# Performance work log

Hardware: AMD Instinct MI355X
Metric: run time of the kernel (lower is better)

Reference implementation:

```python
import jax, jax.numpy as jnp
import numpy as np

B, L, SRC_DIM = 64, 384, 512
HID, EMB = 512, 256
NUM_CLASSES = 250
NUM_STEPS = 127  # batch_max_length(128) - 1


def setup_inputs() -> dict:
    key = jax.random.key(0)
    ks = jax.random.split(key, 13)
    s = 0.05
    return {
        "src": jax.random.normal(ks[0], (B, L, SRC_DIM), jnp.float32),
        "text": jax.random.randint(ks[1], (B, NUM_STEPS), 0, NUM_CLASSES + 1),
        "emb_table": jax.random.normal(ks[2], (NUM_CLASSES + 1, EMB), jnp.float32) * s,
        "Wi2h": jax.random.normal(ks[3], (HID, SRC_DIM), jnp.float32) * s,
        "Wh2h": jax.random.normal(ks[4], (HID, HID), jnp.float32) * s,
        "bh2h": jax.random.normal(ks[5], (HID,), jnp.float32) * s,
        "wscore": jax.random.normal(ks[6], (HID,), jnp.float32) * s,
        "W_ih": jax.random.normal(ks[7], (4 * HID, SRC_DIM + EMB), jnp.float32) * s,
        "b_ih": jax.random.normal(ks[8], (4 * HID,), jnp.float32) * s,
        "W_hh": jax.random.normal(ks[9], (4 * HID, HID), jnp.float32) * s,
        "b_hh": jax.random.normal(ks[10], (4 * HID,), jnp.float32) * s,
        "Wgen": jax.random.normal(ks[11], (NUM_CLASSES, HID), jnp.float32) * s,
        "bgen": jax.random.normal(ks[12], (NUM_CLASSES,), jnp.float32) * s,
    }


def reference(src, text, emb_table, Wi2h, Wh2h, bh2h, wscore,
              W_ih, b_ih, W_hh, b_hh, Wgen, bgen):
    """ASTERDecoder teacher-forced forward (num_layers=1).
    src: [B, L, C]; text: [B, T] int tokens. Returns probs [B, T, num_classes].
    """
    b = src.shape[0]
    H = Wh2h.shape[0]
    # i2h(src) is constant across decode steps -> hoist out of the loop.
    src_feat = jnp.einsum('blc,hc->blh', src, Wi2h)          # [B, L, H]
    emb_seq = emb_table[text]                                # [B, T, E]

    def step(carry, emb_t):
        h, c = carry                                         # [B, H] each
        proj = h @ Wh2h.T + bh2h                             # h2h(prev_hidden)
        # Bahdanau score + softmax over L, then context via weighted sum.
        logit = jnp.tanh(src_feat + proj[:, None, :]) @ wscore   # [B, L]
        alpha = jax.nn.softmax(logit, axis=1)
        context = jnp.einsum('bl,blc->bc', alpha, src)       # [B, C]
        x = jnp.concatenate([context, emb_t], axis=1)        # [B, C+E]
        # LSTMCell gates (PyTorch order: i, f, g, o)
        gates = x @ W_ih.T + b_ih + h @ W_hh.T + b_hh        # [B, 4H]
        i, f, g, o = jnp.split(gates, 4, axis=1)
        i, f, o = jax.nn.sigmoid(i), jax.nn.sigmoid(f), jax.nn.sigmoid(o)
        g = jnp.tanh(g)
        c_new = f * c + i * g
        h_new = o * jnp.tanh(c_new)
        return (h_new, c_new), h_new

    init = (jnp.zeros((b, H), src.dtype), jnp.zeros((b, H), src.dtype))
    _, hs = jax.lax.scan(step, init, jnp.swapaxes(emb_seq, 0, 1))  # hs: [T, B, H]
    output_hiddens = jnp.swapaxes(hs, 0, 1)                  # [B, T, H]
    probs = jnp.einsum('bth,nh->btn', output_hiddens, Wgen) + bgen
    return probs
```

## Files before the change

### kernel.cpp

```cpp
#include <hip/hip_runtime.h>

typedef unsigned short u16;
typedef unsigned int   u32;
typedef _Float16 f16;
typedef f16   f16x2 __attribute__((ext_vector_type(2)));
typedef f16   f16x8 __attribute__((ext_vector_type(8)));
typedef float f32x4 __attribute__((ext_vector_type(4)));
typedef u32   u32x4 __attribute__((ext_vector_type(4)));

#define B_  64
#define L_  384
#define CS  512
#define H_  512
#define E_  256
#define NC  250
#define T_  127
#define XROW 1024

__device__ __forceinline__ float h2f(u16 u){ f16 h; __builtin_memcpy(&h,&u,2); return (float)h; }
__device__ __forceinline__ u16  f2h(float f){ f16 h=(f16)f; u16 u; __builtin_memcpy(&u,&h,2); return u; }
__device__ __forceinline__ float wredsum(float v){
#pragma unroll
  for (int o=32;o>0;o>>=1) v += __shfl_down(v, o, 64);
  return v;
}
__device__ __forceinline__ float tanh_f(float x){
  x = fminf(fmaxf(x, -15.f), 15.f);
  float e = __expf(2.f*x);
  return (e-1.f)/(e+1.f);
}
__device__ __forceinline__ float sigm_f(float x){
  x = fminf(fmaxf(x, -30.f), 30.f);
  return 1.f/(1.f+__expf(-x));
}
__device__ __forceinline__ float dot2f(u32 a, u32 b, float c){
  f16x2 x, y; __builtin_memcpy(&x,&a,4); __builtin_memcpy(&y,&b,4);
#if __has_builtin(__builtin_amdgcn_fdot2)
  return __builtin_amdgcn_fdot2(x, y, c, false);
#else
  return c + (float)x[0]*(float)y[0] + (float)x[1]*(float)y[1];
#endif
}

__global__ __launch_bounds__(256) void k_cvt(const float* __restrict__ in, f16* __restrict__ o, int n){
  int i = blockIdx.x*256 + threadIdx.x;
  if (i < n) o[i] = (f16)in[i];
}

__global__ __launch_bounds__(256) void k_packwhq(const float* __restrict__ Wh, u32* __restrict__ Wq){
  int i = blockIdx.x*256 + threadIdx.x;
  if (i < 64*512*4){
    int kq = i >> 11, n = (i >> 2) & 511, e = i & 3;
    int k = kq*8 + e*2;
    u32 lo = f2h(Wh[(size_t)n*512 + k]);
    u32 hi = f2h(Wh[(size_t)n*512 + k + 1]);
    Wq[i] = lo | (hi<<16);
  }
}

__global__ __launch_bounds__(256) void k_packwg(const float* __restrict__ Wih,
    const float* __restrict__ Whh, const float* __restrict__ bih, const float* __restrict__ bhh,
    f16* __restrict__ Wg, float* __restrict__ bias_g){
  int i = blockIdx.x*256 + threadIdx.x;
  if (i < 2048*1280){
    int p = i / 1280, c = i - p*1280;
    int j = p >> 4, q = p & 15, g = q >> 2, hl = q & 3;
    int r = g*512 + (j<<2) + hl;
    float v = (c < 768) ? Wih[(size_t)r*768 + c] : Whh[(size_t)r*512 + (c-768)];
    Wg[i] = (f16)v;
    if (c == 0) bias_g[p] = bih[r] + bhh[r];
  }
}

__global__ __launch_bounds__(256) void k_emb(const int* __restrict__ text,
    const float* __restrict__ embt, f16* __restrict__ embseq){
  int i = blockIdx.x*256 + threadIdx.x;
  if (i < B_*T_*E_){
    int bt = i >> 8, col = i & 255;
    int tok = text[bt];
    embseq[i] = (f16)embt[(size_t)tok*E_ + col];
  }
}

__global__ __launch_bounds__(256) void k_sf_mfma(
    const float* __restrict__ A, const f16* __restrict__ Wn, u16* __restrict__ sf)
{
  int w = threadIdx.x >> 6, lane = threadIdx.x & 63;
  int quad = lane >> 4, l16 = lane & 15;
  int m0 = blockIdx.x * 64;
  int nb = blockIdx.y * 256 + w * 64;
  const float* ap0 = A  + (size_t)(m0 + l16)*512 + quad*8;
  const f16*   bp0 = Wn + (size_t)(nb + l16)*512 + quad*8;
  f32x4 acc[4][4] = {};
  for (int k0=0; k0<512; k0+=32){
    f16x8 bfr[4];
#pragma unroll
    for (int nt=0; nt<4; nt++)
      bfr[nt] = *(const f16x8*)(bp0 + (size_t)nt*16*512 + k0);
#pragma unroll
    for (int f=0; f<4; f++){
      const float* ap = ap0 + (size_t)f*16*512 + k0;
      float4 a0 = *(const float4*)ap;
      float4 a1 = *(const float4*)(ap+4);
      f16x8 afr = { (f16)a0.x,(f16)a0.y,(f16)a0.z,(f16)a0.w,
                    (f16)a1.x,(f16)a1.y,(f16)a1.z,(f16)a1.w };
#pragma unroll
      for (int nt=0; nt<4; nt++)
        acc[f][nt] = __builtin_amdgcn_mfma_f32_16x16x32_f16(afr, bfr[nt], acc[f][nt], 0,0,0);
    }
  }
#pragma unroll
  for (int f=0; f<4; f++)
#pragma unroll
    for (int nt=0; nt<4; nt++)
#pragma unroll
      for (int r=0; r<4; r++){
        int m = m0 + f*16 + quad*4 + r;
        int n = nb + nt*16 + l16;
        sf[(size_t)m*512 + n] = f2h(acc[f][nt][r]);
      }
}

__global__ __launch_bounds__(256) void gemm_probs(
    const u16* __restrict__ A, const float* __restrict__ W, const float* __restrict__ bias,
    float* __restrict__ Cd, int M, int N, int K)
{
  __shared__ float As[16][64+1];
  __shared__ float Ws[16][64+1];
  const int tid = threadIdx.x;
  const int bm = blockIdx.x*64, bn = blockIdx.y*64;
  const int lr = tid>>2;
  const int lc = (tid&3)*4;
  const int ty = tid>>4, tx = tid&15;
  float acc[4][4];
#pragma unroll
  for (int i=0;i<4;i++)
#pragma unroll
    for (int j=0;j<4;j++) acc[i][j]=0.f;

  for (int k0=0;k0<K;k0+=16){
    ushort4 va = *(const ushort4*)(A + (size_t)(bm+lr)*K + k0 + lc);
    As[lc+0][lr]=h2f(va.x); As[lc+1][lr]=h2f(va.y); As[lc+2][lr]=h2f(va.z); As[lc+3][lr]=h2f(va.w);
    int n = bn + lr;
    if (n < N){
      float4 vw = *(const float4*)(W + (size_t)n*K + k0 + lc);
      Ws[lc+0][lr]=vw.x; Ws[lc+1][lr]=vw.y; Ws[lc+2][lr]=vw.z; Ws[lc+3][lr]=vw.w;
    } else {
      Ws[lc+0][lr]=0.f; Ws[lc+1][lr]=0.f; Ws[lc+2][lr]=0.f; Ws[lc+3][lr]=0.f;
    }
    __syncthreads();
#pragma unroll
    for (int k=0;k<16;k++){
      float a[4], w[4];
#pragma unroll
      for (int i=0;i<4;i++) a[i]=As[k][ty*4+i];
#pragma unroll
      for (int j=0;j<4;j++) w[j]=Ws[k][tx*4+j];
#pragma unroll
      for (int i=0;i<4;i++)
#pragma unroll
        for (int j=0;j<4;j++) acc[i][j] += a[i]*w[j];
    }
    __syncthreads();
  }
#pragma unroll
  for (int i=0;i<4;i++){
    int m = bm + ty*4 + i;
#pragma unroll
    for (int j=0;j<4;j++){
      int n = bn + tx*4 + j;
      if (n < N) Cd[(size_t)m*N + n] = acc[i][j] + bias[n];
    }
  }
}

__global__ __launch_bounds__(512) void k_att1(
    const u32* __restrict__ WhQ, const u16* __restrict__ sf,
    const f16* __restrict__ Xc, const float* __restrict__ bh2h,
    const float* __restrict__ wsc, float* __restrict__ logit)
{
  const int b   = blockIdx.x >> 2;
  const int q   = blockIdx.x & 3;
  const int tid = threadIdx.x;
  const int wid = tid >> 6, lane = tid & 63;

  __shared__ __align__(16) u32 sh_h2[256];
  __shared__ float sh_proj[512];

  if (tid < 256) sh_h2[tid] = ((const u32*)(Xc + (size_t)b*XROW + 512))[tid];
  __syncthreads();

  {
    const u32* wp = WhQ + ((size_t)tid << 2);
    const u32x4* hp = (const u32x4*)sh_h2;
    float a0=0.f, a1=0.f, a2=0.f, a3=0.f;
#pragma unroll 8
    for (int kq=0; kq<64; kq++){
      u32x4 wq = *(const u32x4*)(wp + ((size_t)kq << 11));
      u32x4 hq = hp[kq];
      a0 = dot2f(wq.x, hq.x, a0);
      a1 = dot2f(wq.y, hq.y, a1);
      a2 = dot2f(wq.z, hq.z, a2);
      a3 = dot2f(wq.w, hq.w, a3);
    }
    sh_proj[tid] = (a0+a1) + (a2+a3) + bh2h[tid];
  }
  __syncthreads();

  {
    float pv[8], wv[8];
#pragma unroll
    for (int j=0;j<8;j++){ pv[j]=sh_proj[lane*8+j]; wv[j]=wsc[lane*8+j]; }
    const int l0 = q*96 + wid*12;
    const f16* sp0 = (const f16*)sf + (((size_t)(b*L_ + l0)) << 9) + lane*8;
#pragma unroll 4
    for (int i=0;i<12;i++){
      f16x8 s = *(const f16x8*)(sp0 + ((size_t)i << 9));
      float v;
      v  = tanh_f((float)s[0]+pv[0])*wv[0];
      v += tanh_f((float)s[1]+pv[1])*wv[1];
      v += tanh_f((float)s[2]+pv[2])*wv[2];
      v += tanh_f((float)s[3]+pv[3])*wv[3];
      v += tanh_f((float)s[4]+pv[4])*wv[4];
      v += tanh_f((float)s[5]+pv[5])*wv[5];
      v += tanh_f((float)s[6]+pv[6])*wv[6];
      v += tanh_f((float)s[7]+pv[7])*wv[7];
      v = wredsum(v);
      if (lane == 0) logit[b*L_ + l0 + i] = v;
    }
  }
}

__global__ __launch_bounds__(512) void k_ctx2(
    const float* __restrict__ logit, const f16* __restrict__ src16,
    f16* __restrict__ Xc)
{
  const int b   = blockIdx.x;
  const int tid = threadIdx.x;
  const int wid = tid >> 6, lane = tid & 63;

  __shared__ float sh_al[L_];
  __shared__ float sh_red[16];
  __shared__ float sh_cp[8][512];

  float inv;
  {
    float va = (tid < L_) ? logit[b*L_ + tid] : -3.0e38f;
    float m = va;
#pragma unroll
    for (int o=32;o>0;o>>=1) m = fmaxf(m, __shfl_down(m,o,64));
    if (lane==0) sh_red[wid] = m;
    __syncthreads();
    m = fmaxf(fmaxf(fmaxf(sh_red[0],sh_red[1]),fmaxf(sh_red[2],sh_red[3])),
              fmaxf(fmaxf(sh_red[4],sh_red[5]),fmaxf(sh_red[6],sh_red[7])));
    float e = (tid < L_) ? __expf(va - m) : 0.f;
    if (tid < L_) sh_al[tid] = e;
    float ss = wredsum(e);
    if (lane==0) sh_red[8+wid] = ss;
    __syncthreads();
    inv = 1.f/(((sh_red[8]+sh_red[9])+(sh_red[10]+sh_red[11]))
             + ((sh_red[12]+sh_red[13])+(sh_red[14]+sh_red[15])));
  }

  {
    float acc[8] = {0.f,0.f,0.f,0.f,0.f,0.f,0.f,0.f};
    const f16* sp0 = src16 + (((size_t)(b*L_ + wid*48)) << 9) + lane*8;
    const float* alp = sh_al + wid*48;
#pragma unroll 4
    for (int i=0;i<48;i++){
      f16x8 v = *(const f16x8*)(sp0 + ((size_t)i << 9));
      float al = alp[i];
#pragma unroll
      for (int e=0;e<8;e++) acc[e] += al*(float)v[e];
    }
#pragma unroll
    for (int e=0;e<8;e++) sh_cp[wid][lane*8+e] = acc[e];
  }
  __syncthreads();
  if (tid < 256){
    int c0 = tid*2;
    float v0 = (((sh_cp[0][c0]+sh_cp[1][c0])+(sh_cp[2][c0]+sh_cp[3][c0]))
              + ((sh_cp[4][c0]+sh_cp[5][c0])+(sh_cp[6][c0]+sh_cp[7][c0])))*inv;
    int c1 = c0+1;
    float v1 = (((sh_cp[0][c1]+sh_cp[1][c1])+(sh_cp[2][c1]+sh_cp[3][c1]))
              + ((sh_cp[4][c1]+sh_cp[5][c1])+(sh_cp[6][c1]+sh_cp[7][c1])))*inv;
    u32 o = (u32)f2h(v0) | ((u32)f2h(v1) << 16);
    ((u32*)(Xc + (size_t)b*XROW))[tid] = o;
  }
}

__global__ __launch_bounds__(256) void k_gates(
    const f16* __restrict__ X, const f16* __restrict__ Wg,
    const float* __restrict__ bias_g, const f16* __restrict__ embseq,
    float* __restrict__ cbuf, f16* __restrict__ Xn, u16* __restrict__ hs, int t)
{
  __shared__ float gbuf[64][17];
  const int tid  = threadIdx.x;
  const int wid  = tid >> 6, lane = tid & 63;
  const int quad = lane >> 4, l16 = lane & 15;
  const int j = blockIdx.x;
  const f16* bp   = Wg + (size_t)(j*16 + l16)*1280 + quad*8;
  const int brow  = wid*16 + l16;
  const f16* actx = X + (size_t)brow*XROW + quad*8;
  const f16* aemb = embseq + (((size_t)brow*T_ + t)<<8) + quad*8;
  const f16* ah   = actx + 512;
  f32x4 acc = {};
#pragma unroll
  for (int k0=0;k0<512;k0+=32)
    acc = __builtin_amdgcn_mfma_f32_16x16x32_f16(*(const f16x8*)(actx+k0), *(const f16x8*)(bp+k0), acc, 0,0,0);
#pragma unroll
  for (int k0=0;k0<256;k0+=32)
    acc = __builtin_amdgcn_mfma_f32_16x16x32_f16(*(const f16x8*)(aemb+k0), *(const f16x8*)(bp+512+k0), acc, 0,0,0);
#pragma unroll
  for (int k0=0;k0<512;k0+=32)
    acc = __builtin_amdgcn_mfma_f32_16x16x32_f16(*(const f16x8*)(ah+k0), *(const f16x8*)(bp+768+k0), acc, 0,0,0);
#pragma unroll
  for (int r=0;r<4;r++) gbuf[wid*16 + quad*4 + r][l16] = acc[r];
  __syncthreads();
  const int b = tid >> 2, hl = tid & 3;
  const int hd = j*4 + hl;
  float gi = gbuf[b][ 0+hl] + bias_g[j*16 +  0 + hl];
  float gf = gbuf[b][ 4+hl] + bias_g[j*16 +  4 + hl];
  float gg = gbuf[b][ 8+hl] + bias_g[j*16 +  8 + hl];
  float go = gbuf[b][12+hl] + bias_g[j*16 + 12 + hl];
  float fi=sigm_f(gi), ff=sigm_f(gf), fg=tanh_f(gg), fo=sigm_f(go);
  size_t ci = ((size_t)b<<9) + hd;
  float cn = ff*cbuf[ci] + fi*fg;
  float hn = fo*tanh_f(cn);
  cbuf[ci] = cn;
  Xn[(size_t)b*XROW + 512 + hd] = (f16)hn;
  hs[(((size_t)(b*T_ + t))<<9) + hd] = f2h(hn);
}

extern "C" void kernel_launch(void* const* d_in, const int* in_sizes, int n_in,
                              void* d_out, int out_size, void* d_ws, size_t ws_size,
                              hipStream_t stream)
{
  const float* src   = (const float*)d_in[0];
  const int*   text  = (const int*)d_in[1];
  const float* embt  = (const float*)d_in[2];
  const float* Wi2h  = (const float*)d_in[3];
  const float* Wh2h  = (const float*)d_in[4];
  const float* bh2h  = (const float*)d_in[5];
  const float* wsc   = (const float*)d_in[6];
  const float* W_ih  = (const float*)d_in[7];
  const float* b_ih  = (const float*)d_in[8];
  const float* W_hh  = (const float*)d_in[9];
  const float* b_hh  = (const float*)d_in[10];
  const float* Wgen  = (const float*)d_in[11];
  const float* bgen  = (const float*)d_in[12];
  float* out = (float*)d_out;

  char* p = (char*)d_ws;
  u16*   sfw    = (u16*)p;    p += (size_t)B_*L_*H_*2;
  u16*   hsw    = (u16*)p;    p += (size_t)B_*T_*H_*2;
  f16*   src16  = (f16*)p;    p += (size_t)B_*L_*CS*2;
  u32*   WhQ    = (u32*)p;    p += (size_t)64*512*4*4;
  f16*   Wi2h16 = (f16*)p;    p += (size_t)H_*CS*2;
  f16*   WgF    = (f16*)p;    p += (size_t)2048*1280*2;
  f16*   embseq = (f16*)p;    p += (size_t)B_*T_*E_*2;
  f16*   X0     = (f16*)p;    p += (size_t)B_*XROW*2;
  f16*   X1     = (f16*)p;    p += (size_t)B_*XROW*2;
  float* logitw = (float*)p;  p += (size_t)B_*L_*4;
  float* cbuf   = (float*)p;  p += (size_t)B_*H_*4;
  float* bias_g = (float*)p;  p += (size_t)2048*4;

  hipMemsetAsync(X0,   0, (size_t)B_*XROW*2*2, stream);
  hipMemsetAsync(cbuf, 0, (size_t)B_*H_*4, stream);

  k_cvt    <<<(H_*CS+255)/256,    256, 0, stream>>>(Wi2h, Wi2h16, H_*CS);
  k_cvt    <<<(B_*L_*CS+255)/256, 256, 0, stream>>>(src, src16, B_*L_*CS);
  k_packwhq<<<(64*512*4+255)/256, 256, 0, stream>>>(Wh2h, WhQ);
  k_packwg <<<(2048*1280+255)/256,256, 0, stream>>>(W_ih, W_hh, b_ih, b_hh, WgF, bias_g);
  k_emb    <<<(B_*T_*E_+255)/256, 256, 0, stream>>>(text, embt, embseq);

  k_sf_mfma<<<dim3(384,2), 256, 0, stream>>>(src, Wi2h16, sfw);

  for (int t=0; t<T_; t++){
    f16* Xc = (t & 1) ? X1 : X0;
    f16* Xn = (t & 1) ? X0 : X1;
    k_att1<<<256, 512, 0, stream>>>(WhQ, sfw, Xc, bh2h, wsc, logitw);
    k_ctx2<<<64, 512, 0, stream>>>(logitw, src16, Xc);
    k_gates<<<128, 256, 0, stream>>>(Xc, WgF, bias_g, embseq, cbuf, Xn, hsw, t);
  }

  dim3 g2(B_*T_/64, (NC+63)/64);
  gemm_probs<<<g2, 256, 0, stream>>>(hsw, Wgen, bgen, out, B_*T_, NC, H_);
}
```

Before: 5.016 ms.

## Precompute src@W_ih context projection and fuse step into two kernels

Uses linearity to precompute src projected through the context part of W_ih (a [B,L,2048] f16 tensor), so each step's context contribution to the gates becomes an alpha-weighted sum over that tensor instead of a context vector followed by a GEMM. The h/embedding gate part is computed by extra MFMA blocks inside the attention-logit kernel, which cuts the per-step launches from three to two. In exchange each step streams a 100MB precomputed tensor (four times the src bytes) and needs a much larger workspace, with a fallback to the old path when the workspace is too small.

```diff
diff --git a/kernel.cpp b/kernel.cpp
--- a/kernel.cpp
+++ b/kernel.cpp
@@ -16,6 +16,7 @@
 #define NC  250
 #define T_  127
 #define XROW 1024
+#define XEH  768
 
 __device__ __forceinline__ float h2f(u16 u){ f16 h; __builtin_memcpy(&h,&u,2); return (float)h; }
 __device__ __forceinline__ u16  f2h(float f){ f16 h=(f16)f; u16 u; __builtin_memcpy(&u,&h,2); return u; }
@@ -55,6 +56,28 @@
     u32 lo = f2h(Wh[(size_t)n*512 + k]);
     u32 hi = f2h(Wh[(size_t)n*512 + k + 1]);
     Wq[i] = lo | (hi<<16);
+  }
+}
+
+__global__ __launch_bounds__(256) void k_packwcp(const float* __restrict__ Wih, f16* __restrict__ Wcp){
+  int i = blockIdx.x*256 + threadIdx.x;
+  if (i < 2048*512){
+    int pc = i >> 9, k = i & 511;
+    int r = (pc&3)*512 + (pc>>2);
+    Wcp[i] = (f16)Wih[(size_t)r*768 + k];
+  }
+}
+
+__global__ __launch_bounds__(256) void k_packwgp2(const float* __restrict__ Wih,
+    const float* __restrict__ Whh, const float* __restrict__ bih, const float* __restrict__ bhh,
+    f16* __restrict__ WgP, float* __restrict__ bias_g){
+  int i = blockIdx.x*256 + threadIdx.x;
+  if (i < 2048*768){
+    int pc = i / 768, k = i - pc*768;
+    int r = (pc&3)*512 + (pc>>2);
+    float v = (k < 256) ? Wih[(size_t)r*768 + 512 + k] : Whh[(size_t)r*512 + (k-256)];
+    WgP[i] = (f16)v;
+    if (k == 0) bias_g[pc] = bih[r] + bhh[r];
   }
 }
 
@@ -82,8 +105,13 @@
   }
 }
 
+__global__ __launch_bounds__(128) void k_initeh(const f16* __restrict__ embseq, f16* __restrict__ Xeh){
+  int b = blockIdx.x, tid = threadIdx.x;
+  ((u32*)(Xeh + (size_t)b*XEH))[tid] = ((const u32*)(embseq + ((size_t)(b*T_))*256))[tid];
+}
+
 __global__ __launch_bounds__(256) void k_sf_mfma(
-    const float* __restrict__ A, const f16* __restrict__ Wn, u16* __restrict__ sf)
+    const float* __restrict__ A, const f16* __restrict__ Wn, u16* __restrict__ Cd, int N)
 {
   int w = threadIdx.x >> 6, lane = threadIdx.x & 63;
   int quad = lane >> 4, l16 = lane & 15;
@@ -117,7 +145,7 @@
       for (int r=0; r<4; r++){
         int m = m0 + f*16 + quad*4 + r;
         int n = nb + nt*16 + l16;
-        sf[(size_t)m*512 + n] = f2h(acc[f][nt][r]);
+        Cd[(size_t)m*N + n] = f2h(acc[f][nt][r]);
       }
 }
 
@@ -174,6 +202,157 @@
   }
 }
 
+__global__ __launch_bounds__(512) void k_step1(
+    const u32* __restrict__ WhQ, const u16* __restrict__ sf,
+    const f16* __restrict__ Xeh, const float* __restrict__ bh2h,
+    const float* __restrict__ wsc, float* __restrict__ logit,
+    const f16* __restrict__ WgP, const float* __restrict__ bias_g,
+    float* __restrict__ gpart)
+{
+  const int tid = threadIdx.x;
+  const int wid = tid >> 6, lane = tid & 63;
+  __shared__ __align__(16) u32 sh_h2[256];
+  __shared__ float sh_proj[512];
+
+  if (blockIdx.x < 256){
+    const int b = blockIdx.x >> 2;
+    const int q = blockIdx.x & 3;
+    if (tid < 256) sh_h2[tid] = ((const u32*)(Xeh + (size_t)b*XEH + 256))[tid];
+    __syncthreads();
+    {
+      const u32* wp = WhQ + ((size_t)tid << 2);
+      const u32x4* hp = (const u32x4*)sh_h2;
+      float a0=0.f, a1=0.f, a2=0.f, a3=0.f;
+#pragma unroll 8
+      for (int kq=0; kq<64; kq++){
+        u32x4 wq = *(const u32x4*)(wp + ((size_t)kq << 11));
+        u32x4 hq = hp[kq];
+        a0 = dot2f(wq.x, hq.x, a0);
+        a1 = dot2f(wq.y, hq.y, a1);
+        a2 = dot2f(wq.z, hq.z, a2);
+        a3 = dot2f(wq.w, hq.w, a3);
+      }
+      sh_proj[tid] = (a0+a1) + (a2+a3) + bh2h[tid];
+    }
+    __syncthreads();
+    {
+      float pv[8], wv[8];
+#pragma unroll
+      for (int j=0;j<8;j++){ pv[j]=sh_proj[lane*8+j]; wv[j]=wsc[lane*8+j]; }
+      const int l0 = q*96 + wid*12;
+      const f16* sp0 = (const f16*)sf + (((size_t)(b*L_ + l0)) << 9) + lane*8;
+#pragma unroll 4
+      for (int i=0;i<12;i++){
+        f16x8 s = *(const f16x8*)(sp0 + ((size_t)i << 9));
+        float v;
+        v  = tanh_f((float)s[0]+pv[0])*wv[0];
+        v += tanh_f((float)s[1]+pv[1])*wv[1];
+        v += tanh_f((float)s[2]+pv[2])*wv[2];
+        v += tanh_f((float)s[3]+pv[3])*wv[3];
+        v += tanh_f((float)s[4]+pv[4])*wv[4];
+        v += tanh_f((float)s[5]+pv[5])*wv[5];
+        v += tanh_f((float)s[6]+pv[6])*wv[6];
+        v += tanh_f((float)s[7]+pv[7])*wv[7];
+        v = wredsum(v);
+        if (lane == 0) logit[b*L_ + l0 + i] = v;
+      }
+    }
+  } else {
+    const int j = blockIdx.x - 256;
+    const int quad = lane >> 4, l16 = lane & 15;
+    const int n = j*128 + wid*16 + l16;
+    const f16* bp  = WgP + (size_t)n*768 + quad*8;
+    const f16* ap0 = Xeh + (size_t)l16*XEH + quad*8;
+    f32x4 acc[4] = {};
+    for (int k0=0; k0<768; k0+=32){
+      f16x8 bfr = *(const f16x8*)(bp + k0);
+#pragma unroll
+      for (int f=0; f<4; f++){
+        f16x8 afr = *(const f16x8*)(ap0 + (size_t)f*16*XEH + k0);
+        acc[f] = __builtin_amdgcn_mfma_f32_16x16x32_f16(afr, bfr, acc[f], 0,0,0);
+      }
+    }
+    float bias = bias_g[n];
+#pragma unroll
+    for (int f=0; f<4; f++)
+#pragma unroll
+      for (int r=0; r<4; r++){
+        int b2 = f*16 + quad*4 + r;
+        gpart[(size_t)b2*2048 + n] = acc[f][r] + bias;
+      }
+  }
+}
+
+__global__ __launch_bounds__(512) void k_step2(
+    const float* __restrict__ logit, const u16* __restrict__ sg,
+    const float* __restrict__ gpart, const f16* __restrict__ embseq,
+    float* __restrict__ cbuf, f16* __restrict__ Xeh, u16* __restrict__ hs, int t)
+{
+  const int b = blockIdx.x >> 2, q = blockIdx.x & 3;
+  const int tid = threadIdx.x;
+  const int wid = tid >> 6, lane = tid & 63;
+  __shared__ float sh_al[L_];
+  __shared__ float sh_red[16];
+  __shared__ float sh_gs[2][512];
+
+  float inv;
+  {
+    float va = (tid < L_) ? logit[b*L_ + tid] : -3.0e38f;
+    float m = va;
+#pragma unroll
+    for (int o=32;o>0;o>>=1) m = fmaxf(m, __shfl_down(m,o,64));
+    if (lane==0) sh_red[wid] = m;
+    __syncthreads();
+    m = fmaxf(fmaxf(fmaxf(sh_red[0],sh_red[1]),fmaxf(sh_red[2],sh_red[3])),
+              fmaxf(fmaxf(sh_red[4],sh_red[5]),fmaxf(sh_red[6],sh_red[7])));
+    float e = (tid < L_) ? __expf(va - m) : 0.f;
+    if (tid < L_) sh_al[tid] = e;
+    float ss = wredsum(e);
+    if (lane==0) sh_red[8+wid] = ss;
+    __syncthreads();
+    inv = 1.f/(((sh_red[8]+sh_red[9])+(sh_red[10]+sh_red[11]))
+             + ((sh_red[12]+sh_red[13])+(sh_red[14]+sh_red[15])));
+  }
+
+  {
+    const int cp = tid & 255, lh = tid >> 8;
+    const u32* sp = (const u32*)sg + ((size_t)(b*L_ + lh*192))*1024 + q*256 + cp;
+    const float* alp = sh_al + lh*192;
+    float a0 = 0.f, a1 = 0.f;
+#pragma unroll 8
+    for (int l=0;l<192;l++){
+      u32 v = sp[(size_t)l*1024];
+      f16x2 p2; __builtin_memcpy(&p2,&v,4);
+      float al = alp[l];
+      a0 += al*(float)p2[0];
+      a1 += al*(float)p2[1];
+    }
+    sh_gs[lh][cp*2  ] = a0;
+    sh_gs[lh][cp*2+1] = a1;
+  }
+  __syncthreads();
+
+  if (tid < 128){
+    const float4 gp = *(const float4*)(gpart + (size_t)b*2048 + q*512 + tid*4);
+    float gi = (sh_gs[0][tid*4+0] + sh_gs[1][tid*4+0])*inv + gp.x;
+    float gf = (sh_gs[0][tid*4+1] + sh_gs[1][tid*4+1])*inv + gp.y;
+    float gg = (sh_gs[0][tid*4+2] + sh_gs[1][tid*4+2])*inv + gp.z;
+    float go = (sh_gs[0][tid*4+3] + sh_gs[1][tid*4+3])*inv + gp.w;
+    float fi=sigm_f(gi), ff=sigm_f(gf), fg=tanh_f(gg), fo=sigm_f(go);
+    const int hd = q*128 + tid;
+    size_t ci = ((size_t)b<<9) + hd;
+    float cn = ff*cbuf[ci] + fi*fg;
+    float hn = fo*tanh_f(cn);
+    cbuf[ci] = cn;
+    Xeh[(size_t)b*XEH + 256 + hd] = (f16)hn;
+    hs[((size_t)(b*T_ + t))*512 + hd] = f2h(hn);
+  } else if (q == 0 && tid >= 256 && tid < 384 && (t+1) < T_){
+    int c = tid - 256;
+    ((u32*)(Xeh + (size_t)b*XEH))[c] =
+        ((const u32*)(embseq + ((size_t)(b*T_ + t + 1))*256))[c];
+  }
+}
+
 __global__ __launch_bounds__(512) void k_att1(
     const u32* __restrict__ WhQ, const u16* __restrict__ sf,
     const f16* __restrict__ Xc, const float* __restrict__ bh2h,
@@ -183,13 +362,10 @@
   const int q   = blockIdx.x & 3;
   const int tid = threadIdx.x;
   const int wid = tid >> 6, lane = tid & 63;
-
   __shared__ __align__(16) u32 sh_h2[256];
   __shared__ float sh_proj[512];
-
   if (tid < 256) sh_h2[tid] = ((const u32*)(Xc + (size_t)b*XROW + 512))[tid];
   __syncthreads();
-
   {
     const u32* wp = WhQ + ((size_t)tid << 2);
     const u32x4* hp = (const u32x4*)sh_h2;
@@ -206,7 +382,6 @@
     sh_proj[tid] = (a0+a1) + (a2+a3) + bh2h[tid];
   }
   __syncthreads();
-
   {
     float pv[8], wv[8];
 #pragma unroll
@@ -238,11 +413,9 @@
   const int b   = blockIdx.x;
   const int tid = threadIdx.x;
   const int wid = tid >> 6, lane = tid & 63;
-
   __shared__ float sh_al[L_];
   __shared__ float sh_red[16];
   __shared__ float sh_cp[8][512];
-
   float inv;
   {
     float va = (tid < L_) ? logit[b*L_ + tid] : -3.0e38f;
@@ -261,7 +434,6 @@
     inv = 1.f/(((sh_red[8]+sh_red[9])+(sh_red[10]+sh_red[11]))
              + ((sh_red[12]+sh_red[13])+(sh_red[14]+sh_red[15])));
   }
-
   {
     float acc[8] = {0.f,0.f,0.f,0.f,0.f,0.f,0.f,0.f};
     const f16* sp0 = src16 + (((size_t)(b*L_ + wid*48)) << 9) + lane*8;
@@ -351,39 +523,81 @@
   const float* bgen  = (const float*)d_in[12];
   float* out = (float*)d_out;
 
-  char* p = (char*)d_ws;
-  u16*   sfw    = (u16*)p;    p += (size_t)B_*L_*H_*2;
-  u16*   hsw    = (u16*)p;    p += (size_t)B_*T_*H_*2;
-  f16*   src16  = (f16*)p;    p += (size_t)B_*L_*CS*2;
-  u32*   WhQ    = (u32*)p;    p += (size_t)64*512*4*4;
-  f16*   Wi2h16 = (f16*)p;    p += (size_t)H_*CS*2;
-  f16*   WgF    = (f16*)p;    p += (size_t)2048*1280*2;
-  f16*   embseq = (f16*)p;    p += (size_t)B_*T_*E_*2;
-  f16*   X0     = (f16*)p;    p += (size_t)B_*XROW*2;
-  f16*   X1     = (f16*)p;    p += (size_t)B_*XROW*2;
-  float* logitw = (float*)p;  p += (size_t)B_*L_*4;
-  float* cbuf   = (float*)p;  p += (size_t)B_*H_*4;
-  float* bias_g = (float*)p;  p += (size_t)2048*4;
-
-  hipMemsetAsync(X0,   0, (size_t)B_*XROW*2*2, stream);
-  hipMemsetAsync(cbuf, 0, (size_t)B_*H_*4, stream);
-
-  k_cvt    <<<(H_*CS+255)/256,    256, 0, stream>>>(Wi2h, Wi2h16, H_*CS);
-  k_cvt    <<<(B_*L_*CS+255)/256, 256, 0, stream>>>(src, src16, B_*L_*CS);
-  k_packwhq<<<(64*512*4+255)/256, 256, 0, stream>>>(Wh2h, WhQ);
-  k_packwg <<<(2048*1280+255)/256,256, 0, stream>>>(W_ih, W_hh, b_ih, b_hh, WgF, bias_g);
-  k_emb    <<<(B_*T_*E_+255)/256, 256, 0, stream>>>(text, embt, embseq);
-
-  k_sf_mfma<<<dim3(384,2), 256, 0, stream>>>(src, Wi2h16, sfw);
-
-  for (int t=0; t<T_; t++){
-    f16* Xc = (t & 1) ? X1 : X0;
-    f16* Xn = (t & 1) ? X0 : X1;
-    k_att1<<<256, 512, 0, stream>>>(WhQ, sfw, Xc, bh2h, wsc, logitw);
-    k_ctx2<<<64, 512, 0, stream>>>(logitw, src16, Xc);
-    k_gates<<<128, 256, 0, stream>>>(Xc, WgF, bias_g, embseq, cbuf, Xn, hsw, t);
-  }
-
-  dim3 g2(B_*T_/64, (NC+63)/64);
-  gemm_probs<<<g2, 256, 0, stream>>>(hsw, Wgen, bgen, out, B_*T_, NC, H_);
-}
+  const size_t NEED_NEW = (size_t)25165824 + 8323072 + 100663296 + 524288 + 524288
+                        + 2097152 + 3145728 + 4161536 + 98304 + 98304 + 524288
+                        + 131072 + 8192;
+
+  if (ws_size >= NEED_NEW){
+    char* p = (char*)d_ws;
+    u16*   sfw    = (u16*)p;    p += (size_t)B_*L_*H_*2;
+    u16*   hsw    = (u16*)p;    p += (size_t)B_*T_*H_*2;
+    u16*   sg     = (u16*)p;    p += (size_t)B_*L_*2048*2;
+    u32*   WhQ    = (u32*)p;    p += (size_t)64*512*4*4;
+    f16*   Wi2h16 = (f16*)p;    p += (size_t)H_*CS*2;
+    f16*   Wcp    = (f16*)p;    p += (size_t)2048*512*2;
+    f16*   WgP    = (f16*)p;    p += (size_t)2048*768*2;
+    f16*   embseq = (f16*)p;    p += (size_t)B_*T_*E_*2;
+    f16*   Xeh    = (f16*)p;    p += (size_t)B_*XEH*2;
+    float* logitw = (float*)p;  p += (size_t)B_*L_*4;
+    float* gpart  = (float*)p;  p += (size_t)B_*2048*4;
+    float* cbuf   = (float*)p;  p += (size_t)B_*H_*4;
+    float* bias_g = (float*)p;  p += (size_t)2048*4;
+
+    hipMemsetAsync(Xeh,  0, (size_t)B_*XEH*2, stream);
+    hipMemsetAsync(cbuf, 0, (size_t)B_*H_*4, stream);
+
+    k_cvt     <<<(H_*CS+255)/256,    256, 0, stream>>>(Wi2h, Wi2h16, H_*CS);
+    k_packwhq <<<(64*512*4+255)/256, 256, 0, stream>>>(Wh2h, WhQ);
+    k_packwcp <<<(2048*512+255)/256, 256, 0, stream>>>(W_ih, Wcp);
+    k_packwgp2<<<(2048*768+255)/256, 256, 0, stream>>>(W_ih, W_hh, b_ih, b_hh, WgP, bias_g);
+    k_emb     <<<(B_*T_*E_+255)/256, 256, 0, stream>>>(text, embt, embseq);
+    k_initeh  <<<B_, 128, 0, stream>>>(embseq, Xeh);
+
+    k_sf_mfma<<<dim3(384,2), 256, 0, stream>>>(src, Wi2h16, sfw, 512);
+    k_sf_mfma<<<dim3(384,8), 256, 0, stream>>>(src, Wcp,    sg,  2048);
+
+    for (int t=0; t<T_; t++){
+      k_step1<<<272, 512, 0, stream>>>(WhQ, sfw, Xeh, bh2h, wsc, logitw, WgP, bias_g, gpart);
+      k_step2<<<256, 512, 0, stream>>>(logitw, sg, gpart, embseq, cbuf, Xeh, hsw, t);
+    }
+
+    dim3 g2(B_*T_/64, (NC+63)/64);
+    gemm_probs<<<g2, 256, 0, stream>>>(hsw, Wgen, bgen, out, B_*T_, NC, H_);
+  } else {
+    char* p = (char*)d_ws;
+    u16*   sfw    = (u16*)p;    p += (size_t)B_*L_*H_*2;
+    u16*   hsw    = (u16*)p;    p += (size_t)B_*T_*H_*2;
+    f16*   src16  = (f16*)p;    p += (size_t)B_*L_*CS*2;
+    u32*   WhQ    = (u32*)p;    p += (size_t)64*512*4*4;
+    f16*   Wi2h16 = (f16*)p;    p += (size_t)H_*CS*2;
+    f16*   WgF    = (f16*)p;    p += (size_t)2048*1280*2;
+    f16*   embseq = (f16*)p;    p += (size_t)B_*T_*E_*2;
+    f16*   X0     = (f16*)p;    p += (size_t)B_*XROW*2;
+    f16*   X1     = (f16*)p;    p += (size_t)B_*XROW*2;
+    float* logitw = (float*)p;  p += (size_t)B_*L_*4;
+    float* cbuf   = (float*)p;  p += (size_t)B_*H_*4;
+    float* bias_g = (float*)p;  p += (size_t)2048*4;
+
+    hipMemsetAsync(X0,   0, (size_t)B_*XROW*2*2, stream);
+    hipMemsetAsync(cbuf, 0, (size_t)B_*H_*4, stream);
+
+    k_cvt    <<<(H_*CS+255)/256,    256, 0, stream>>>(Wi2h, Wi2h16, H_*CS);
+    k_cvt    <<<(B_*L_*CS+255)/256, 256, 0, stream>>>(src, src16, B_*L_*CS);
+    k_packwhq<<<(64*512*4+255)/256, 256, 0, stream>>>(Wh2h, WhQ);
+    k_packwg <<<(2048*1280+255)/256,256, 0, stream>>>(W_ih, W_hh, b_ih, b_hh, WgF, bias_g);
+    k_emb    <<<(B_*T_*E_+255)/256, 256, 0, stream>>>(text, embt, embseq);
+
+    k_sf_mfma<<<dim3(384,2), 256, 0, stream>>>(src, Wi2h16, sfw, 512);
+
+    for (int t=0; t<T_; t++){
+      f16* Xc = (t & 1) ? X1 : X0;
+      f16* Xn = (t & 1) ? X0 : X1;
+      k_att1<<<256, 512, 0, stream>>>(WhQ, sfw, Xc, bh2h, wsc, logitw);
+      k_ctx2<<<64, 512, 0, stream>>>(logitw, src16, Xc);
+      k_gates<<<128, 256, 0, stream>>>(Xc, WgF, bias_g, embseq, cbuf, Xn, hsw, t);
+    }
+
+    dim3 g2(B_*T_/64, (NC+63)/64);
+    gemm_probs<<<g2, 256, 0, stream>>>(hsw, Wgen, bgen, out, B_*T_, NC, H_);
+  }
+}
```

After: 6.815 ms. +35.9%, slower.

## Fuse attention and context per step, overlap emb/h gate GEMM, MFMA output projection

Applied to the files above, without the earlier changes.

Each decode step drops from three kernels to two. The first kernel runs score, exp and partial context per quarter of L, and in the same launch extra blocks compute the embedding and hidden gate contributions. The second reduces the partial contexts and denominators, applies the context gate GEMM and the LSTM cell. The softmax max pass is replaced by a fixed shift of 20, which removes one global reduction but relies on logits staying within a bounded range to avoid overflow or underflow. The final probability GEMM moves from a scalar fp32 tiled kernel to fp16 MFMA.

```diff
diff --git a/kernel.cpp b/kernel.cpp
--- a/kernel.cpp
+++ b/kernel.cpp
@@ -15,7 +15,7 @@
 #define E_  256
 #define NC  250
 #define T_  127
-#define XROW 1024
+#define MSHIFT 20.0f
 
 __device__ __forceinline__ float h2f(u16 u){ f16 h; __builtin_memcpy(&h,&u,2); return (float)h; }
 __device__ __forceinline__ u16  f2h(float f){ f16 h=(f16)f; u16 u; __builtin_memcpy(&u,&h,2); return u; }
@@ -58,17 +58,25 @@
   }
 }
 
-__global__ __launch_bounds__(256) void k_packwg(const float* __restrict__ Wih,
+__global__ __launch_bounds__(256) void k_packwcp(const float* __restrict__ Wih, f16* __restrict__ Wcp){
+  int i = blockIdx.x*256 + threadIdx.x;
+  if (i < 2048*512){
+    int pc = i >> 9, k = i & 511;
+    int r = (pc&3)*512 + (pc>>2);
+    Wcp[i] = (f16)Wih[(size_t)r*768 + k];
+  }
+}
+
+__global__ __launch_bounds__(256) void k_packwgp2(const float* __restrict__ Wih,
     const float* __restrict__ Whh, const float* __restrict__ bih, const float* __restrict__ bhh,
-    f16* __restrict__ Wg, float* __restrict__ bias_g){
+    f16* __restrict__ WgP, float* __restrict__ bias_g){
   int i = blockIdx.x*256 + threadIdx.x;
-  if (i < 2048*1280){
-    int p = i / 1280, c = i - p*1280;
-    int j = p >> 4, q = p & 15, g = q >> 2, hl = q & 3;
-    int r = g*512 + (j<<2) + hl;
-    float v = (c < 768) ? Wih[(size_t)r*768 + c] : Whh[(size_t)r*512 + (c-768)];
-    Wg[i] = (f16)v;
-    if (c == 0) bias_g[p] = bih[r] + bhh[r];
+  if (i < 2048*768){
+    int pc = i / 768, k = i - pc*768;
+    int r = (pc&3)*512 + (pc>>2);
+    float v = (k < 256) ? Wih[(size_t)r*768 + 512 + k] : Whh[(size_t)r*512 + (k-256)];
+    WgP[i] = (f16)v;
+    if (k == 0) bias_g[pc] = bih[r] + bhh[r];
   }
 }
 
@@ -83,7 +91,7 @@
 }
 
 __global__ __launch_bounds__(256) void k_sf_mfma(
-    const float* __restrict__ A, const f16* __restrict__ Wn, u16* __restrict__ sf)
+    const float* __restrict__ A, const f16* __restrict__ Wn, u16* __restrict__ Cd, int N)
 {
   int w = threadIdx.x >> 6, lane = threadIdx.x & 63;
   int quad = lane >> 4, l16 = lane & 15;
@@ -117,219 +125,236 @@
       for (int r=0; r<4; r++){
         int m = m0 + f*16 + quad*4 + r;
         int n = nb + nt*16 + l16;
-        sf[(size_t)m*512 + n] = f2h(acc[f][nt][r]);
-      }
-}
-
-__global__ __launch_bounds__(256) void gemm_probs(
-    const u16* __restrict__ A, const float* __restrict__ W, const float* __restrict__ bias,
-    float* __restrict__ Cd, int M, int N, int K)
+        Cd[(size_t)m*N + n] = f2h(acc[f][nt][r]);
+      }
+}
+
+__global__ __launch_bounds__(256) void k_probs_mfma(
+    const u16* __restrict__ A, const f16* __restrict__ Wn,
+    const float* __restrict__ bias, float* __restrict__ Cd)
 {
-  __shared__ float As[16][64+1];
-  __shared__ float Ws[16][64+1];
-  const int tid = threadIdx.x;
-  const int bm = blockIdx.x*64, bn = blockIdx.y*64;
-  const int lr = tid>>2;
-  const int lc = (tid&3)*4;
-  const int ty = tid>>4, tx = tid&15;
-  float acc[4][4];
-#pragma unroll
-  for (int i=0;i<4;i++)
-#pragma unroll
-    for (int j=0;j<4;j++) acc[i][j]=0.f;
-
-  for (int k0=0;k0<K;k0+=16){
-    ushort4 va = *(const ushort4*)(A + (size_t)(bm+lr)*K + k0 + lc);
-    As[lc+0][lr]=h2f(va.x); As[lc+1][lr]=h2f(va.y); As[lc+2][lr]=h2f(va.z); As[lc+3][lr]=h2f(va.w);
-    int n = bn + lr;
-    if (n < N){
-      float4 vw = *(const float4*)(W + (size_t)n*K + k0 + lc);
-      Ws[lc+0][lr]=vw.x; Ws[lc+1][lr]=vw.y; Ws[lc+2][lr]=vw.z; Ws[lc+3][lr]=vw.w;
-    } else {
-      Ws[lc+0][lr]=0.f; Ws[lc+1][lr]=0.f; Ws[lc+2][lr]=0.f; Ws[lc+3][lr]=0.f;
-    }
-    __syncthreads();
-#pragma unroll
-    for (int k=0;k<16;k++){
-      float a[4], w[4];
-#pragma unroll
-      for (int i=0;i<4;i++) a[i]=As[k][ty*4+i];
-#pragma unroll
-      for (int j=0;j<4;j++) w[j]=Ws[k][tx*4+j];
-#pragma unroll
-      for (int i=0;i<4;i++)
-#pragma unroll
-        for (int j=0;j<4;j++) acc[i][j] += a[i]*w[j];
-    }
-    __syncthreads();
-  }
-#pragma unroll
-  for (int i=0;i<4;i++){
-    int m = bm + ty*4 + i;
-#pragma unroll
-    for (int j=0;j<4;j++){
-      int n = bn + tx*4 + j;
-      if (n < N) Cd[(size_t)m*N + n] = acc[i][j] + bias[n];
-    }
-  }
-}
-
-__global__ __launch_bounds__(512) void k_att1(
+  int w = threadIdx.x >> 6, lane = threadIdx.x & 63;
+  int quad = lane >> 4, l16 = lane & 15;
+  int m0 = blockIdx.x * 64;
+  int nb = w * 64;
+  const f16* ap0 = (const f16*)A + (size_t)(m0 + l16)*512 + quad*8;
+  const f16* bp0 = Wn + (size_t)(nb + l16)*512 + quad*8;
+  f32x4 acc[4][4] = {};
+  for (int k0=0; k0<512; k0+=32){
+    f16x8 bfr[4];
+#pragma unroll
+    for (int nt=0; nt<4; nt++)
+      bfr[nt] = *(const f16x8*)(bp0 + (size_t)nt*16*512 + k0);
+#pragma unroll
+    for (int f=0; f<4; f++){
+      f16x8 afr = *(const f16x8*)(ap0 + (size_t)f*16*512 + k0);
+#pragma unroll
+      for (int nt=0; nt<4; nt++)
+        acc[f][nt] = __builtin_amdgcn_mfma_f32_16x16x32_f16(afr, bfr[nt], acc[f][nt], 0,0,0);
+    }
+  }
+#pragma unroll
+  for (int f=0; f<4; f++)
+#pragma unroll
+    for (int nt=0; nt<4; nt++)
+#pragma unroll
+      for (int r=0; r<4; r++){
+        int m = m0 + f*16 + quad*4 + r;
+        int n = nb + nt*16 + l16;
+        if (n < NC) Cd[(size_t)m*NC + n] = acc[f][nt][r] + bias[n];
+      }
+}
+
+__global__ __launch_bounds__(512) void k_stepA(
     const u32* __restrict__ WhQ, const u16* __restrict__ sf,
-    const f16* __restrict__ Xc, const float* __restrict__ bh2h,
-    const float* __restrict__ wsc, float* __restrict__ logit)
+    const f16* __restrict__ src16, const f16* __restrict__ hbuf,
+    const float* __restrict__ bh2h, const float* __restrict__ wsc,
+    const f16* __restrict__ WgP, const float* __restrict__ bias_g,
+    const f16* __restrict__ embseq,
+    float* __restrict__ ctxp, float* __restrict__ denp,
+    float* __restrict__ gpart, int t)
 {
-  const int b   = blockIdx.x >> 2;
-  const int q   = blockIdx.x & 3;
   const int tid = threadIdx.x;
   const int wid = tid >> 6, lane = tid & 63;
 
-  __shared__ __align__(16) u32 sh_h2[256];
-  __shared__ float sh_proj[512];
-
-  if (tid < 256) sh_h2[tid] = ((const u32*)(Xc + (size_t)b*XROW + 512))[tid];
-  __syncthreads();
-
-  {
-    const u32* wp = WhQ + ((size_t)tid << 2);
-    const u32x4* hp = (const u32x4*)sh_h2;
-    float a0=0.f, a1=0.f, a2=0.f, a3=0.f;
+  if (blockIdx.x < 256){
+    const int b = blockIdx.x >> 2;
+    const int q = blockIdx.x & 3;
+    __shared__ __align__(16) u32 sh_h2[256];
+    __shared__ float sh_proj[512];
+    __shared__ float sh_e[96];
+    __shared__ float sh_cp[8][512];
+
+    if (tid < 256) sh_h2[tid] = ((const u32*)(hbuf + (size_t)b*512))[tid];
+    __syncthreads();
+    {
+      const u32* wp = WhQ + ((size_t)tid << 2);
+      const u32x4* hp = (const u32x4*)sh_h2;
+      float a0=0.f, a1=0.f, a2=0.f, a3=0.f;
 #pragma unroll 8
-    for (int kq=0; kq<64; kq++){
-      u32x4 wq = *(const u32x4*)(wp + ((size_t)kq << 11));
-      u32x4 hq = hp[kq];
-      a0 = dot2f(wq.x, hq.x, a0);
-      a1 = dot2f(wq.y, hq.y, a1);
-      a2 = dot2f(wq.z, hq.z, a2);
-      a3 = dot2f(wq.w, hq.w, a3);
-    }
-    sh_proj[tid] = (a0+a1) + (a2+a3) + bh2h[tid];
-  }
-  __syncthreads();
-
-  {
-    float pv[8], wv[8];
-#pragma unroll
-    for (int j=0;j<8;j++){ pv[j]=sh_proj[lane*8+j]; wv[j]=wsc[lane*8+j]; }
-    const int l0 = q*96 + wid*12;
-    const f16* sp0 = (const f16*)sf + (((size_t)(b*L_ + l0)) << 9) + lane*8;
+      for (int kq=0; kq<64; kq++){
+        u32x4 wq = *(const u32x4*)(wp + ((size_t)kq << 11));
+        u32x4 hq = hp[kq];
+        a0 = dot2f(wq.x, hq.x, a0);
+        a1 = dot2f(wq.y, hq.y, a1);
+        a2 = dot2f(wq.z, hq.z, a2);
+        a3 = dot2f(wq.w, hq.w, a3);
+      }
+      sh_proj[tid] = (a0+a1) + (a2+a3) + bh2h[tid];
+    }
+    __syncthreads();
+    {
+      float pv[8], wv[8];
+#pragma unroll
+      for (int j=0;j<8;j++){ pv[j]=sh_proj[lane*8+j]; wv[j]=wsc[lane*8+j]; }
+      const int l0 = q*96 + wid*12;
+      const f16* sp0 = (const f16*)sf + (((size_t)(b*L_ + l0)) << 9) + lane*8;
 #pragma unroll 4
-    for (int i=0;i<12;i++){
-      f16x8 s = *(const f16x8*)(sp0 + ((size_t)i << 9));
-      float v;
-      v  = tanh_f((float)s[0]+pv[0])*wv[0];
-      v += tanh_f((float)s[1]+pv[1])*wv[1];
-      v += tanh_f((float)s[2]+pv[2])*wv[2];
-      v += tanh_f((float)s[3]+pv[3])*wv[3];
-      v += tanh_f((float)s[4]+pv[4])*wv[4];
-      v += tanh_f((float)s[5]+pv[5])*wv[5];
-      v += tanh_f((float)s[6]+pv[6])*wv[6];
-      v += tanh_f((float)s[7]+pv[7])*wv[7];
+      for (int i=0;i<12;i++){
+        f16x8 s = *(const f16x8*)(sp0 + ((size_t)i << 9));
+        float v;
+        v  = tanh_f((float)s[0]+pv[0])*wv[0];
+        v += tanh_f((float)s[1]+pv[1])*wv[1];
+        v += tanh_f((float)s[2]+pv[2])*wv[2];
+        v += tanh_f((float)s[3]+pv[3])*wv[3];
+        v += tanh_f((float)s[4]+pv[4])*wv[4];
+        v += tanh_f((float)s[5]+pv[5])*wv[5];
+        v += tanh_f((float)s[6]+pv[6])*wv[6];
+        v += tanh_f((float)s[7]+pv[7])*wv[7];
+        v = wredsum(v);
+        if (lane == 0) sh_e[wid*12 + i] = __expf(v - MSHIFT);
+      }
+    }
+    __syncthreads();
+    if (wid == 0){
+      float v = sh_e[lane] + (lane < 32 ? sh_e[64+lane] : 0.f);
       v = wredsum(v);
-      if (lane == 0) logit[b*L_ + l0 + i] = v;
-    }
-  }
-}
-
-__global__ __launch_bounds__(512) void k_ctx2(
-    const float* __restrict__ logit, const f16* __restrict__ src16,
-    f16* __restrict__ Xc)
+      if (lane == 0) denp[q*64 + b] = v;
+    }
+    {
+      float acc[8] = {0.f,0.f,0.f,0.f,0.f,0.f,0.f,0.f};
+      const f16* sp0 = src16 + (((size_t)(b*L_ + q*96 + wid*12)) << 9) + lane*8;
+      const float* alp = sh_e + wid*12;
+#pragma unroll 4
+      for (int i=0;i<12;i++){
+        f16x8 v = *(const f16x8*)(sp0 + ((size_t)i << 9));
+        float al = alp[i];
+#pragma unroll
+        for (int e=0;e<8;e++) acc[e] += al*(float)v[e];
+      }
+#pragma unroll
+      for (int e=0;e<8;e++) sh_cp[wid][lane*8+e] = acc[e];
+    }
+    __syncthreads();
+    if (tid < 256){
+      int c0 = tid*2;
+      float v0 = (((sh_cp[0][c0]+sh_cp[1][c0])+(sh_cp[2][c0]+sh_cp[3][c0]))
+                + ((sh_cp[4][c0]+sh_cp[5][c0])+(sh_cp[6][c0]+sh_cp[7][c0])));
+      int c1 = c0+1;
+      float v1 = (((sh_cp[0][c1]+sh_cp[1][c1])+(sh_cp[2][c1]+sh_cp[3][c1]))
+                + ((sh_cp[4][c1]+sh_cp[5][c1])+(sh_cp[6][c1]+sh_cp[7][c1])));
+      float2 o; o.x = v0; o.y = v1;
+      *(float2*)(ctxp + (((size_t)(q*64 + b)) << 9) + c0) = o;
+    }
+  } else {
+    const int j = blockIdx.x - 256;
+    const int quad = lane >> 4, l16 = lane & 15;
+    const int n = j*128 + wid*16 + l16;
+    const f16* bp = WgP + (size_t)n*768 + quad*8;
+    f32x4 acc[4] = {};
+    for (int k0=0; k0<256; k0+=32){
+      f16x8 bfr = *(const f16x8*)(bp + k0);
+#pragma unroll
+      for (int f=0; f<4; f++){
+        int br = f*16 + l16;
+        f16x8 afr = *(const f16x8*)(embseq + (((size_t)(br*T_ + t)) << 8) + quad*8 + k0);
+        acc[f] = __builtin_amdgcn_mfma_f32_16x16x32_f16(afr, bfr, acc[f], 0,0,0);
+      }
+    }
+    for (int k0=0; k0<512; k0+=32){
+      f16x8 bfr = *(const f16x8*)(bp + 256 + k0);
+#pragma unroll
+      for (int f=0; f<4; f++){
+        int br = f*16 + l16;
+        f16x8 afr = *(const f16x8*)(hbuf + (size_t)br*512 + quad*8 + k0);
+        acc[f] = __builtin_amdgcn_mfma_f32_16x16x32_f16(afr, bfr, acc[f], 0,0,0);
+      }
+    }
+    float bias = bias_g[n];
+#pragma unroll
+    for (int f=0; f<4; f++)
+#pragma unroll
+      for (int r=0; r<4; r++){
+        int b2 = f*16 + quad*4 + r;
+        gpart[((size_t)b2 << 11) + n] = acc[f][r] + bias;
+      }
+  }
+}
+
+__global__ __launch_bounds__(256) void k_stepB(
+    const float* __restrict__ ctxp, const float* __restrict__ denp,
+    const float* __restrict__ gpart, const f16* __restrict__ Wcp,
+    float* __restrict__ cbuf, f16* __restrict__ hbuf, u16* __restrict__ hs, int t)
 {
-  const int b   = blockIdx.x;
+  __shared__ f16   sh_ctx[64][520];
+  __shared__ float gbuf[64][17];
+  __shared__ float sh_inv[64];
   const int tid = threadIdx.x;
   const int wid = tid >> 6, lane = tid & 63;
-
-  __shared__ float sh_al[L_];
-  __shared__ float sh_red[16];
-  __shared__ float sh_cp[8][512];
-
-  float inv;
-  {
-    float va = (tid < L_) ? logit[b*L_ + tid] : -3.0e38f;
-    float m = va;
-#pragma unroll
-    for (int o=32;o>0;o>>=1) m = fmaxf(m, __shfl_down(m,o,64));
-    if (lane==0) sh_red[wid] = m;
-    __syncthreads();
-    m = fmaxf(fmaxf(fmaxf(sh_red[0],sh_red[1]),fmaxf(sh_red[2],sh_red[3])),
-              fmaxf(fmaxf(sh_red[4],sh_red[5]),fmaxf(sh_red[6],sh_red[7])));
-    float e = (tid < L_) ? __expf(va - m) : 0.f;
-    if (tid < L_) sh_al[tid] = e;
-    float ss = wredsum(e);
-    if (lane==0) sh_red[8+wid] = ss;
-    __syncthreads();
-    inv = 1.f/(((sh_red[8]+sh_red[9])+(sh_red[10]+sh_red[11]))
-             + ((sh_red[12]+sh_red[13])+(sh_red[14]+sh_red[15])));
-  }
-
-  {
-    float acc[8] = {0.f,0.f,0.f,0.f,0.f,0.f,0.f,0.f};
-    const f16* sp0 = src16 + (((size_t)(b*L_ + wid*48)) << 9) + lane*8;
-    const float* alp = sh_al + wid*48;
-#pragma unroll 4
-    for (int i=0;i<48;i++){
-      f16x8 v = *(const f16x8*)(sp0 + ((size_t)i << 9));
-      float al = alp[i];
-#pragma unroll
-      for (int e=0;e<8;e++) acc[e] += al*(float)v[e];
-    }
-#pragma unroll
-    for (int e=0;e<8;e++) sh_cp[wid][lane*8+e] = acc[e];
-  }
-  __syncthreads();
-  if (tid < 256){
-    int c0 = tid*2;
-    float v0 = (((sh_cp[0][c0]+sh_cp[1][c0])+(sh_cp[2][c0]+sh_cp[3][c0]))
-              + ((sh_cp[4][c0]+sh_cp[5][c0])+(sh_cp[6][c0]+sh_cp[7][c0])))*inv;
-    int c1 = c0+1;
-    float v1 = (((sh_cp[0][c1]+sh_cp[1][c1])+(sh_cp[2][c1]+sh_cp[3][c1]))
-              + ((sh_cp[4][c1]+sh_cp[5][c1])+(sh_cp[6][c1]+sh_cp[7][c1])))*inv;
-    u32 o = (u32)f2h(v0) | ((u32)f2h(v1) << 16);
-    ((u32*)(Xc + (size_t)b*XROW))[tid] = o;
-  }
-}
-
-__global__ __launch_bounds__(256) void k_gates(
-    const f16* __restrict__ X, const f16* __restrict__ Wg,
-    const float* __restrict__ bias_g, const f16* __restrict__ embseq,
-    float* __restrict__ cbuf, f16* __restrict__ Xn, u16* __restrict__ hs, int t)
-{
-  __shared__ float gbuf[64][17];
-  const int tid  = threadIdx.x;
-  const int wid  = tid >> 6, lane = tid & 63;
   const int quad = lane >> 4, l16 = lane & 15;
   const int j = blockIdx.x;
-  const f16* bp   = Wg + (size_t)(j*16 + l16)*1280 + quad*8;
-  const int brow  = wid*16 + l16;
-  const f16* actx = X + (size_t)brow*XROW + quad*8;
-  const f16* aemb = embseq + (((size_t)brow*T_ + t)<<8) + quad*8;
-  const f16* ah   = actx + 512;
-  f32x4 acc = {};
-#pragma unroll
-  for (int k0=0;k0<512;k0+=32)
-    acc = __builtin_amdgcn_mfma_f32_16x16x32_f16(*(const f16x8*)(actx+k0), *(const f16x8*)(bp+k0), acc, 0,0,0);
-#pragma unroll
-  for (int k0=0;k0<256;k0+=32)
-    acc = __builtin_amdgcn_mfma_f32_16x16x32_f16(*(const f16x8*)(aemb+k0), *(const f16x8*)(bp+512+k0), acc, 0,0,0);
-#pragma unroll
-  for (int k0=0;k0<512;k0+=32)
-    acc = __builtin_amdgcn_mfma_f32_16x16x32_f16(*(const f16x8*)(ah+k0), *(const f16x8*)(bp+768+k0), acc, 0,0,0);
-#pragma unroll
-  for (int r=0;r<4;r++) gbuf[wid*16 + quad*4 + r][l16] = acc[r];
+
+  if (tid < 64)
+    sh_inv[tid] = 1.f/(((denp[tid] + denp[64+tid]) + (denp[128+tid] + denp[192+tid])));
   __syncthreads();
-  const int b = tid >> 2, hl = tid & 3;
-  const int hd = j*4 + hl;
-  float gi = gbuf[b][ 0+hl] + bias_g[j*16 +  0 + hl];
-  float gf = gbuf[b][ 4+hl] + bias_g[j*16 +  4 + hl];
-  float gg = gbuf[b][ 8+hl] + bias_g[j*16 +  8 + hl];
-  float go = gbuf[b][12+hl] + bias_g[j*16 + 12 + hl];
-  float fi=sigm_f(gi), ff=sigm_f(gf), fg=tanh_f(gg), fo=sigm_f(go);
-  size_t ci = ((size_t)b<<9) + hd;
-  float cn = ff*cbuf[ci] + fi*fg;
-  float hn = fo*tanh_f(cn);
-  cbuf[ci] = cn;
-  Xn[(size_t)b*XROW + 512 + hd] = (f16)hn;
-  hs[(((size_t)(b*T_ + t))<<9) + hd] = f2h(hn);
+
+#pragma unroll 4
+  for (int i=0;i<32;i++){
+    int flat = tid + i*256;
+    int b = flat >> 7, c4 = flat & 127;
+    const float* base = ctxp + ((size_t)b << 9) + (c4 << 2);
+    float4 v0 = *(const float4*)(base);
+    float4 v1 = *(const float4*)(base + (64<<9));
+    float4 v2 = *(const float4*)(base + (128<<9));
+    float4 v3 = *(const float4*)(base + (192<<9));
+    float inv = sh_inv[b];
+    int c = c4*4;
+    sh_ctx[b][c+0] = (f16)(((v0.x+v1.x)+(v2.x+v3.x))*inv);
+    sh_ctx[b][c+1] = (f16)(((v0.y+v1.y)+(v2.y+v3.y))*inv);
+    sh_ctx[b][c+2] = (f16)(((v0.z+v1.z)+(v2.z+v3.z))*inv);
+    sh_ctx[b][c+3] = (f16)(((v0.w+v1.w)+(v2.w+v3.w))*inv);
+  }
+  __syncthreads();
+
+  {
+    const f16* bp = Wcp + (size_t)(j*16 + l16)*512 + quad*8;
+    const f16* ap = &sh_ctx[wid*16 + l16][quad*8];
+    f32x4 acc = {};
+#pragma unroll
+    for (int k0=0; k0<512; k0+=32)
+      acc = __builtin_amdgcn_mfma_f32_16x16x32_f16(*(const f16x8*)(ap + k0),
+                                                   *(const f16x8*)(bp + k0), acc, 0,0,0);
+#pragma unroll
+    for (int r=0;r<4;r++) gbuf[wid*16 + quad*4 + r][l16] = acc[r];
+  }
+  __syncthreads();
+
+  {
+    const int b2 = tid >> 2, hl = tid & 3;
+    const int hd = j*4 + hl;
+    float4 gp = *(const float4*)(gpart + ((size_t)b2 << 11) + (size_t)hd*4);
+    float gi = gbuf[b2][hl*4+0] + gp.x;
+    float gf = gbuf[b2][hl*4+1] + gp.y;
+    float gg = gbuf[b2][hl*4+2] + gp.z;
+    float go = gbuf[b2][hl*4+3] + gp.w;
+    float fi=sigm_f(gi), ff=sigm_f(gf), fg=tanh_f(gg), fo=sigm_f(go);
+    size_t ci = ((size_t)b2 << 9) + hd;
+    float cn = ff*cbuf[ci] + fi*fg;
+    float hn = fo*tanh_f(cn);
+    cbuf[ci] = cn;
+    hbuf[((size_t)b2 << 9) + hd] = (f16)hn;
+    hs[((size_t)(b2*T_ + t)) * 512 + hd] = f2h(hn);
+  }
 }
 
 extern "C" void kernel_launch(void* const* d_in, const int* in_sizes, int n_in,
@@ -357,33 +382,36 @@
   f16*   src16  = (f16*)p;    p += (size_t)B_*L_*CS*2;
   u32*   WhQ    = (u32*)p;    p += (size_t)64*512*4*4;
   f16*   Wi2h16 = (f16*)p;    p += (size_t)H_*CS*2;
-  f16*   WgF    = (f16*)p;    p += (size_t)2048*1280*2;
+  f16*   Wcp    = (f16*)p;    p += (size_t)2048*512*2;
+  f16*   WgP    = (f16*)p;    p += (size_t)2048*768*2;
+  f16*   Wgen16 = (f16*)p;    p += (size_t)256*512*2;
   f16*   embseq = (f16*)p;    p += (size_t)B_*T_*E_*2;
-  f16*   X0     = (f16*)p;    p += (size_t)B_*XROW*2;
-  f16*   X1     = (f16*)p;    p += (size_t)B_*XROW*2;
-  float* logitw = (float*)p;  p += (size_t)B_*L_*4;
+  f16*   hbuf   = (f16*)p;    p += (size_t)B_*H_*2;
+  float* ctxp   = (float*)p;  p += (size_t)4*B_*512*4;
+  float* denp   = (float*)p;  p += (size_t)256*4;
+  float* gpart  = (float*)p;  p += (size_t)B_*2048*4;
   float* cbuf   = (float*)p;  p += (size_t)B_*H_*4;
   float* bias_g = (float*)p;  p += (size_t)2048*4;
 
-  hipMemsetAsync(X0,   0, (size_t)B_*XROW*2*2, stream);
-  hipMemsetAsync(cbuf, 0, (size_t)B_*H_*4, stream);
-
-  k_cvt    <<<(H_*CS+255)/256,    256, 0, stream>>>(Wi2h, Wi2h16, H_*CS);
-  k_cvt    <<<(B_*L_*CS+255)/256, 256, 0, stream>>>(src, src16, B_*L_*CS);
-  k_packwhq<<<(64*512*4+255)/256, 256, 0, stream>>>(Wh2h, WhQ);
-  k_packwg <<<(2048*1280+255)/256,256, 0, stream>>>(W_ih, W_hh, b_ih, b_hh, WgF, bias_g);
-  k_emb    <<<(B_*T_*E_+255)/256, 256, 0, stream>>>(text, embt, embseq);
-
-  k_sf_mfma<<<dim3(384,2), 256, 0, stream>>>(src, Wi2h16, sfw);
+  hipMemsetAsync(hbuf,   0, (size_t)B_*H_*2, stream);
+  hipMemsetAsync(cbuf,   0, (size_t)B_*H_*4, stream);
+  hipMemsetAsync(Wgen16, 0, (size_t)256*512*2, stream);
+
+  k_cvt     <<<(H_*CS+255)/256,    256, 0, stream>>>(Wi2h, Wi2h16, H_*CS);
+  k_cvt     <<<(B_*L_*CS+255)/256, 256, 0, stream>>>(src, src16, B_*L_*CS);
+  k_cvt     <<<(NC*512+255)/256,   256, 0, stream>>>(Wgen, (f16*)Wgen16, NC*512);
+  k_packwhq <<<(64*512*4+255)/256, 256, 0, stream>>>(Wh2h, WhQ);
+  k_packwcp <<<(2048*512+255)/256, 256, 0, stream>>>(W_ih, Wcp);
+  k_packwgp2<<<(2048*768+255)/256, 256, 0, stream>>>(W_ih, W_hh, b_ih, b_hh, WgP, bias_g);
+  k_emb     <<<(B_*T_*E_+255)/256, 256, 0, stream>>>(text, embt, embseq);
+
+  k_sf_mfma<<<dim3(384,2), 256, 0, stream>>>(src, Wi2h16, sfw, 512);
 
   for (int t=0; t<T_; t++){
-    f16* Xc = (t & 1) ? X1 : X0;
-    f16* Xn = (t & 1) ? X0 : X1;
-    k_att1<<<256, 512, 0, stream>>>(WhQ, sfw, Xc, bh2h, wsc, logitw);
-    k_ctx2<<<64, 512, 0, stream>>>(logitw, src16, Xc);
-    k_gates<<<128, 256, 0, stream>>>(Xc, WgF, bias_g, embseq, cbuf, Xn, hsw, t);
-  }
-
-  dim3 g2(B_*T_/64, (NC+63)/64);
-  gemm_probs<<<g2, 256, 0, stream>>>(hsw, Wgen, bgen, out, B_*T_, NC, H_);
-}
+    k_stepA<<<272, 512, 0, stream>>>(WhQ, sfw, src16, hbuf, bh2h, wsc,
+                                     WgP, bias_g, embseq, ctxp, denp, gpart, t);
+    k_stepB<<<128, 256, 0, stream>>>(ctxp, denp, gpart, Wcp, cbuf, hbuf, hsw, t);
+  }
+
+  k_probs_mfma<<<127, 256, 0, stream>>>(hsw, Wgen16, bgen, out);
+}
```

New measurement: 6.085 ms. 1.21x slower.
